# Kernel tuning notes

Hardware: AMD Instinct MI355X
Metric: run time of the kernel (lower is better)

The kernel has to match this reference:

```python
import jax, jax.numpy as jnp
import numpy as np

N, T, DIN, DH = 100000, 512, 256, 256


def setup_inputs() -> dict:
    key = jax.random.key(0)
    ks = jax.random.split(key, 7)
    s_in = 1.0 / np.sqrt(DH)  # torch GRU init scale
    X = jax.random.normal(ks[0], (N, DIN), dtype=jnp.float32)
    H = (jax.random.uniform(ks[1], (N, T)) < 0.02).astype(jnp.float32)
    W_ih = jax.random.uniform(ks[2], (3 * DH, DIN), minval=-s_in, maxval=s_in, dtype=jnp.float32)
    W_hh = jax.random.uniform(ks[3], (3 * DH, DH), minval=-s_in, maxval=s_in, dtype=jnp.float32)
    b_ih = jax.random.uniform(ks[4], (3 * DH,), minval=-s_in, maxval=s_in, dtype=jnp.float32)
    b_hh = jax.random.uniform(ks[5], (3 * DH,), minval=-s_in, maxval=s_in, dtype=jnp.float32)
    w_att = jax.random.uniform(ks[6], (DH,), minval=-s_in, maxval=s_in, dtype=jnp.float32)
    return {"X": X, "H": H, "W_ih": W_ih, "W_hh": W_hh, "b_ih": b_ih, "b_hh": b_hh, "w_att": w_att}


def _gru(visit_emb, W_ih, W_hh, b_ih, b_hh):
    # torch GRU gate order: r, z, n
    dh = W_hh.shape[1]
    gx = visit_emb @ W_ih.T + b_ih  # [T, 3H] precomputed input projections

    def step(h, gx_t):
        gh = h @ W_hh.T + b_hh  # [3H]
        r = jax.nn.sigmoid(gx_t[:dh] + gh[:dh])
        z = jax.nn.sigmoid(gx_t[dh:2 * dh] + gh[dh:2 * dh])
        n = jnp.tanh(gx_t[2 * dh:] + r * gh[2 * dh:])
        h_new = (1.0 - z) * n + z * h
        return h_new, h_new

    h0 = jnp.zeros((dh,), dtype=visit_emb.dtype)
    _, hs = jax.lax.scan(step, h0, gx)
    return hs  # [T, H]


def reference(X, H, W_ih, W_hh, b_ih, b_hh, w_att):
    visit_emb = H.T @ X  # [T, Din] incidence aggregation
    hidden = _gru(visit_emb, W_ih, W_hh, b_ih, b_hh)  # [T, H]
    alpha = jax.nn.softmax(hidden @ w_att, axis=0)  # [T]
    # diag(alpha) @ hidden summed over T == alpha-weighted sum
    return jnp.einsum("t,th->h", alpha, hidden)
```

## Files before the change

kernel.cpp:

```cpp
#include <hip/hip_runtime.h>
#include <hip/hip_bf16.h>

#define N_ROWS 100000
#define T_DIM  512
#define DIN    256
#define DH     256
#define KC     800
#define NSTEP  25
#define NCHUNK 125

typedef __attribute__((ext_vector_type(8))) short s16x8;
typedef __attribute__((ext_vector_type(4))) float f32x4;

static __device__ __forceinline__ unsigned bf16pair(float lo, float hi) {
  unsigned a = __builtin_bit_cast(unsigned, lo);
  unsigned b = __builtin_bit_cast(unsigned, hi);
  a = (a + 0x7fffu + ((a >> 16) & 1u)) >> 16;
  b = (b + 0x7fffu + ((b >> 16) & 1u)) & 0xffff0000u;
  return a | b;
}

__global__ __launch_bounds__(512, 2) void k_agg_mfma(
    const float* __restrict__ X, const float* __restrict__ Hm,
    float* __restrict__ ve, float* __restrict__ ve_part, int use_part)
{
  __shared__ unsigned smem[8192];
  const int tid  = threadIdx.x;
  const int mt   = blockIdx.x & 1;
  const int kc   = blockIdx.x >> 1;
  const int m0   = mt * 256;
  const int k0   = kc * KC;
  const int lane = tid & 63;
  const int wv   = tid >> 6;
  const int wm   = wv >> 2, wn = wv & 3;

  f32x4 acc[8][4] = {};

  const int kp0 = tid >> 6;
  const int kp1 = kp0 + 8;
  const int gg  = tid & 63;

  float4 ra0, ra1, ra2, ra3, rb0, rb1, rb2, rb3;

  auto load_tile = [&](int kt) {
    const size_t kb = (size_t)(k0 + kt * 32);
    const float* pa0 = &Hm[(kb + 2 * kp0) * T_DIM + m0 + gg * 4];
    ra0 = *(const float4*)pa0;
    ra1 = *(const float4*)(pa0 + T_DIM);
    const float* pa1 = &Hm[(kb + 2 * kp1) * T_DIM + m0 + gg * 4];
    ra2 = *(const float4*)pa1;
    ra3 = *(const float4*)(pa1 + T_DIM);
    const float* pb0 = &X[(kb + 2 * kp0) * DIN + gg * 4];
    rb0 = *(const float4*)pb0;
    rb1 = *(const float4*)(pb0 + DIN);
    const float* pb1 = &X[(kb + 2 * kp1) * DIN + gg * 4];
    rb2 = *(const float4*)pb1;
    rb3 = *(const float4*)(pb1 + DIN);
  };

  auto store_tile = [&]() {
#pragma unroll
    for (int d = 0; d < 4; ++d) {
      const int m  = gg * 4 + d;
      const int sw = d << 2;
      smem[m * 16 + (kp0 ^ sw)]        = bf16pair(((const float*)&ra0)[d], ((const float*)&ra1)[d]);
      smem[m * 16 + (kp1 ^ sw)]        = bf16pair(((const float*)&ra2)[d], ((const float*)&ra3)[d]);
      smem[4096 + m * 16 + (kp0 ^ sw)] = bf16pair(((const float*)&rb0)[d], ((const float*)&rb1)[d]);
      smem[4096 + m * 16 + (kp1 ^ sw)] = bf16pair(((const float*)&rb2)[d], ((const float*)&rb3)[d]);
    }
  };

  auto compute = [&]() {
    const uint4* sv = (const uint4*)smem;
    s16x8 af[8], bfr[4];
#pragma unroll
    for (int fm = 0; fm < 8; ++fm) {
      const int m = wm * 128 + fm * 16 + (lane & 15);
      af[fm] = __builtin_bit_cast(s16x8, sv[m * 4 + ((lane >> 4) ^ (m & 3))]);
    }
#pragma unroll
    for (int fn = 0; fn < 4; ++fn) {
      const int n = wn * 64 + fn * 16 + (lane & 15);
      bfr[fn] = __builtin_bit_cast(s16x8, sv[1024 + n * 4 + ((lane >> 4) ^ (n & 3))]);
    }
#pragma unroll
    for (int fm = 0; fm < 8; ++fm)
#pragma unroll
      for (int fn = 0; fn < 4; ++fn)
        acc[fm][fn] = __builtin_amdgcn_mfma_f32_16x16x32_bf16(af[fm], bfr[fn], acc[fm][fn], 0, 0, 0);
  };

  load_tile(0);
  store_tile();
  for (int kt = 0; kt < NSTEP; ++kt) {
    __syncthreads();
    if (kt + 1 < NSTEP) load_tile(kt + 1);
    compute();
    __syncthreads();
    if (kt + 1 < NSTEP) store_tile();
  }

  if (use_part) {
    float* dst = ve_part + (size_t)kc * (512 * 256);
#pragma unroll
    for (int fm = 0; fm < 8; ++fm) {
      const int r0 = m0 + wm * 128 + fm * 16 + (lane >> 4) * 4;
#pragma unroll
      for (int fn = 0; fn < 4; ++fn) {
        const int cc = wn * 64 + fn * 16 + (lane & 15);
#pragma unroll
        for (int q = 0; q < 4; ++q)
          dst[(size_t)(r0 + q) * 256 + cc] = acc[fm][fn][q];
      }
    }
  } else {
#pragma unroll
    for (int fm = 0; fm < 8; ++fm) {
      const int r0 = m0 + wm * 128 + fm * 16 + (lane >> 4) * 4;
#pragma unroll
      for (int fn = 0; fn < 4; ++fn) {
        const int cc = wn * 64 + fn * 16 + (lane & 15);
#pragma unroll
        for (int q = 0; q < 4; ++q)
          atomicAdd(&ve[(size_t)(r0 + q) * 256 + cc], acc[fm][fn][q]);
      }
    }
  }
}

__global__ __launch_bounds__(256) void k_gx(
    const float* __restrict__ vesrc, int npart,
    const float* __restrict__ Wih, const float* __restrict__ bih,
    float* __restrict__ gx)
{
  __shared__ float vl[DIN];
  const int t = blockIdx.x, j = threadIdx.x;
  float s = 0.f;
  for (int p = 0; p < npart; ++p) s += vesrc[(size_t)p * (512 * 256) + t * DIN + j];
  vl[j] = s;
  __syncthreads();
  float a0 = bih[j], a1 = bih[256 + j], a2 = bih[512 + j];
  const float* __restrict__ w0 = &Wih[(size_t)j * DIN];
  const float* __restrict__ w1 = &Wih[(size_t)(j + 256) * DIN];
  const float* __restrict__ w2 = &Wih[(size_t)(j + 512) * DIN];
#pragma unroll 4
  for (int k = 0; k < DIN; ++k) {
    const float v = vl[k];
    a0 = fmaf(w0[k], v, a0);
    a1 = fmaf(w1[k], v, a1);
    a2 = fmaf(w2[k], v, a2);
  }
  gx[t * 768 + j]       = a0;
  gx[t * 768 + 256 + j] = a1;
  gx[t * 768 + 512 + j] = a2;
}

__global__ __launch_bounds__(512, 2) __attribute__((amdgpu_waves_per_eu(2, 2)))
void k_gru_att(
    const float* __restrict__ Whh, const float* __restrict__ bhh,
    const float* __restrict__ gx, const float* __restrict__ watt,
    float* __restrict__ hs, float* __restrict__ out)
{
  __shared__ __hip_bfloat16 hb[DH];
  __shared__ float ghs[768];
  __shared__ float bsh[768];
  __shared__ float sc[T_DIM];
  __shared__ float red[2];

  const int tid = threadIdx.x;
  const int w   = tid >> 6;
  const int l   = tid & 63;
  const int lr  = l & 15;
  const int lg  = l >> 4;

  int rowbase[6];
  rowbase[0] = w * 32;       rowbase[1] = w * 32 + 16;
  rowbase[2] = 256 + w * 32; rowbase[3] = 256 + w * 32 + 16;
  rowbase[4] = 512 + w * 32; rowbase[5] = 512 + w * 32 + 16;

  s16x8 wf[6][8];
#pragma unroll
  for (int tt = 0; tt < 6; ++tt) {
    const float* rp = &Whh[(size_t)(rowbase[tt] + lr) * DH + lg * 8];
#pragma unroll
    for (int kb = 0; kb < 8; ++kb) {
      const float4 x0 = *(const float4*)(rp + kb * 32);
      const float4 x1 = *(const float4*)(rp + kb * 32 + 4);
      uint4 uu;
      uu.x = bf16pair(x0.x, x0.y);
      uu.y = bf16pair(x0.z, x0.w);
      uu.z = bf16pair(x1.x, x1.y);
      uu.w = bf16pair(x1.z, x1.w);
      wf[tt][kb] = __builtin_bit_cast(s16x8, uu);
    }
  }

  bsh[tid] = bhh[tid < 768 ? tid : 0];
  if (tid < 256) {
    bsh[512 + tid] = bhh[512 + tid];
    hb[tid] = __float2bfloat16(0.0f);
  }
  float h = 0.f;
  __syncthreads();

  for (int t = 0; t < T_DIM; ++t) {
    float gxr = 0.f, gxz = 0.f, gxn = 0.f;
    if (tid < 256) {
      gxr = gx[t * 768 + tid];
      gxz = gx[t * 768 + 256 + tid];
      gxn = gx[t * 768 + 512 + tid];
    }
    f32x4 acc[6];
#pragma unroll
    for (int tt = 0; tt < 6; ++tt)
      acc[tt] = *(const f32x4*)&bsh[rowbase[tt] + lg * 4];
#pragma unroll
    for (int kb = 0; kb < 8; ++kb) {
      const s16x8 bf = *(const s16x8*)((const char*)hb + kb * 64 + lg * 16);
#pragma unroll
      for (int tt = 0; tt < 6; ++tt)
        acc[tt] = __builtin_amdgcn_mfma_f32_16x16x32_bf16(wf[tt][kb], bf, acc[tt], 0, 0, 0);
    }
    if (lr == 0) {
#pragma unroll
      for (int tt = 0; tt < 6; ++tt)
        *(f32x4*)&ghs[rowbase[tt] + lg * 4] = acc[tt];
    }
    __syncthreads();
    if (tid < 256) {
      const float r = 1.f / (1.f + __expf(-(gxr + ghs[tid])));
      const float z = 1.f / (1.f + __expf(-(gxz + ghs[256 + tid])));
      const float pn = gxn + r * ghs[512 + tid];
      const float n = 2.f / (1.f + __expf(-2.f * pn)) - 1.f;
      h = (1.f - z) * n + z * h;
      hs[t * DH + tid] = h;
      hb[tid] = __float2bfloat16(h);
    }
    __syncthreads();
  }

  {
    const float* __restrict__ hr = &hs[tid * DH];
    float s = 0.f;
#pragma unroll 4
    for (int k = 0; k < DH; k += 4) {
      const float4 hv = *(const float4*)(hr + k);
      const float4 wv4 = *(const float4*)(watt + k);
      s = fmaf(hv.x, wv4.x, s); s = fmaf(hv.y, wv4.y, s);
      s = fmaf(hv.z, wv4.z, s); s = fmaf(hv.w, wv4.w, s);
    }
    sc[tid] = s;
  }
  __syncthreads();
  if (tid < 64) {
    float m = -1e30f;
#pragma unroll
    for (int i = 0; i < 8; ++i) m = fmaxf(m, sc[tid * 8 + i]);
#pragma unroll
    for (int off = 32; off > 0; off >>= 1) m = fmaxf(m, __shfl_down(m, off));
    if (tid == 0) red[0] = m;
  }
  __syncthreads();
  const float M = red[0];
  sc[tid] = __expf(sc[tid] - M);
  __syncthreads();
  if (tid < 64) {
    float s = 0.f;
#pragma unroll
    for (int i = 0; i < 8; ++i) s += sc[tid * 8 + i];
#pragma unroll
    for (int off = 32; off > 0; off >>= 1) s += __shfl_down(s, off);
    if (tid == 0) red[1] = s;
  }
  __syncthreads();
  const float inv = 1.f / red[1];
  {
    const int j = tid & 255, half = tid >> 8;
    float acc = 0.f;
    for (int t = half * 256; t < half * 256 + 256; ++t)
      acc = fmaf(sc[t], hs[t * DH + j], acc);
    bsh[half * 256 + j] = acc;
  }
  __syncthreads();
  if (tid < 256) out[tid] = (bsh[tid] + bsh[256 + tid]) * inv;
}

extern "C" void kernel_launch(void* const* d_in, const int* in_sizes, int n_in,
                              void* d_out, int out_size, void* d_ws, size_t ws_size,
                              hipStream_t stream) {
  const float* X    = (const float*)d_in[0];
  const float* H    = (const float*)d_in[1];
  const float* Wih  = (const float*)d_in[2];
  const float* Whh  = (const float*)d_in[3];
  const float* bih  = (const float*)d_in[4];
  const float* bhh  = (const float*)d_in[5];
  const float* watt = (const float*)d_in[6];
  float* out = (float*)d_out;

  char* ws = (char*)d_ws;
  float* gx      = (float*)ws;
  float* hs      = (float*)(ws + 1572864);
  float* ve      = (float*)(ws + 2097152);
  float* ve_part = (float*)(ws + 2621440);

  const size_t need_part = 2621440 + 65536000;
  const int use_part = (ws_size >= need_part) ? 1 : 0;

  if (!use_part)
    hipMemsetAsync(ve, 0, T_DIM * DIN * sizeof(float), stream);

  k_agg_mfma<<<2 * NCHUNK, 512, 0, stream>>>(X, H, ve, ve_part, use_part);
  k_gx<<<T_DIM, 256, 0, stream>>>(use_part ? ve_part : ve, use_part ? NCHUNK : 1,
                                  Wih, bih, gx);
  k_gru_att<<<1, 512, 0, stream>>>(Whh, bhh, gx, watt, hs, out);
}
```

Before: 1.030 ms.

## Shrink GRU recurrence block to 4 waves with 12 MFMA tiles each

The sequential GRU kernel now runs with 256 threads (4 waves) instead of 512. Each wave holds 12 bf16 weight tiles of W_hh in registers rather than 6, and every thread does the gate math, with no idle half-block. The goal is to cut barrier and synchronisation cost per timestep in the latency-bound 512-step loop and to give the compiler a one-wave-per-SIMD register budget. The trade-off is more serial MFMA work per wave per step and a larger register footprint, plus w_att is staged in shared memory for the attention epilogue.

Result: slower. 1.177 ms (+14.2%).

```diff
diff --git a/kernel.cpp b/kernel.cpp
--- a/kernel.cpp
+++ b/kernel.cpp
@@ -155,7 +155,8 @@
   gx[t * 768 + 512 + j] = a2;
 }
 
-__global__ __launch_bounds__(512, 2) __attribute__((amdgpu_waves_per_eu(2, 2)))
+__global__ __attribute__((amdgpu_flat_work_group_size(256, 256),
+                          amdgpu_waves_per_eu(1, 1)))
 void k_gru_att(
     const float* __restrict__ Whh, const float* __restrict__ bhh,
     const float* __restrict__ gx, const float* __restrict__ watt,
@@ -165,6 +166,7 @@
   __shared__ float ghs[768];
   __shared__ float bsh[768];
   __shared__ float sc[T_DIM];
+  __shared__ float wa[DH];
   __shared__ float red[2];
 
   const int tid = threadIdx.x;
@@ -173,61 +175,60 @@
   const int lr  = l & 15;
   const int lg  = l >> 4;
 
-  int rowbase[6];
-  rowbase[0] = w * 32;       rowbase[1] = w * 32 + 16;
-  rowbase[2] = 256 + w * 32; rowbase[3] = 256 + w * 32 + 16;
-  rowbase[4] = 512 + w * 32; rowbase[5] = 512 + w * 32 + 16;
-
-  s16x8 wf[6][8];
-#pragma unroll
-  for (int tt = 0; tt < 6; ++tt) {
-    const float* rp = &Whh[(size_t)(rowbase[tt] + lr) * DH + lg * 8];
-#pragma unroll
-    for (int kb = 0; kb < 8; ++kb) {
-      const float4 x0 = *(const float4*)(rp + kb * 32);
-      const float4 x1 = *(const float4*)(rp + kb * 32 + 4);
-      uint4 uu;
-      uu.x = bf16pair(x0.x, x0.y);
-      uu.y = bf16pair(x0.z, x0.w);
-      uu.z = bf16pair(x1.x, x1.y);
-      uu.w = bf16pair(x1.z, x1.w);
-      wf[tt][kb] = __builtin_bit_cast(s16x8, uu);
-    }
-  }
-
-  bsh[tid] = bhh[tid < 768 ? tid : 0];
-  if (tid < 256) {
-    bsh[512 + tid] = bhh[512 + tid];
-    hb[tid] = __float2bfloat16(0.0f);
-  }
+  s16x8 wf[12][8];
+#pragma unroll
+  for (int g = 0; g < 3; ++g) {
+#pragma unroll
+    for (int s = 0; s < 4; ++s) {
+      const float* rp = &Whh[(size_t)(g * 256 + w * 64 + s * 16 + lr) * DH + lg * 8];
+#pragma unroll
+      for (int kb = 0; kb < 8; ++kb) {
+        const float4 x0 = *(const float4*)(rp + kb * 32);
+        const float4 x1 = *(const float4*)(rp + kb * 32 + 4);
+        uint4 uu;
+        uu.x = bf16pair(x0.x, x0.y);
+        uu.y = bf16pair(x0.z, x0.w);
+        uu.z = bf16pair(x1.x, x1.y);
+        uu.w = bf16pair(x1.z, x1.w);
+        wf[g * 4 + s][kb] = __builtin_bit_cast(s16x8, uu);
+      }
+    }
+  }
+
+  bsh[tid] = bhh[tid];
+  bsh[256 + tid] = bhh[256 + tid];
+  bsh[512 + tid] = bhh[512 + tid];
+  hb[tid] = __float2bfloat16(0.0f);
+  wa[tid] = watt[tid];
   float h = 0.f;
   __syncthreads();
 
   for (int t = 0; t < T_DIM; ++t) {
-    float gxr = 0.f, gxz = 0.f, gxn = 0.f;
-    if (tid < 256) {
-      gxr = gx[t * 768 + tid];
-      gxz = gx[t * 768 + 256 + tid];
-      gxn = gx[t * 768 + 512 + tid];
-    }
-    f32x4 acc[6];
-#pragma unroll
-    for (int tt = 0; tt < 6; ++tt)
-      acc[tt] = *(const f32x4*)&bsh[rowbase[tt] + lg * 4];
+    const float gxr = gx[t * 768 + tid];
+    const float gxz = gx[t * 768 + 256 + tid];
+    const float gxn = gx[t * 768 + 512 + tid];
+    f32x4 acc[12];
+#pragma unroll
+    for (int g = 0; g < 3; ++g)
+#pragma unroll
+      for (int s = 0; s < 4; ++s)
+        acc[g * 4 + s] = *(const f32x4*)&bsh[g * 256 + w * 64 + s * 16 + lg * 4];
 #pragma unroll
     for (int kb = 0; kb < 8; ++kb) {
       const s16x8 bf = *(const s16x8*)((const char*)hb + kb * 64 + lg * 16);
 #pragma unroll
-      for (int tt = 0; tt < 6; ++tt)
+      for (int tt = 0; tt < 12; ++tt)
         acc[tt] = __builtin_amdgcn_mfma_f32_16x16x32_bf16(wf[tt][kb], bf, acc[tt], 0, 0, 0);
     }
     if (lr == 0) {
 #pragma unroll
-      for (int tt = 0; tt < 6; ++tt)
-        *(f32x4*)&ghs[rowbase[tt] + lg * 4] = acc[tt];
+      for (int g = 0; g < 3; ++g)
+#pragma unroll
+        for (int s = 0; s < 4; ++s)
+          *(f32x4*)&ghs[g * 256 + w * 64 + s * 16 + lg * 4] = acc[g * 4 + s];
     }
     __syncthreads();
-    if (tid < 256) {
+    {
       const float r = 1.f / (1.f + __expf(-(gxr + ghs[tid])));
       const float z = 1.f / (1.f + __expf(-(gxz + ghs[256 + tid])));
       const float pn = gxn + r * ghs[512 + tid];
@@ -239,17 +240,19 @@
     __syncthreads();
   }
 
-  {
-    const float* __restrict__ hr = &hs[tid * DH];
+#pragma unroll
+  for (int tt = 0; tt < 2; ++tt) {
+    const int t = tid + tt * 256;
+    const float* __restrict__ hr = &hs[(size_t)t * DH];
     float s = 0.f;
 #pragma unroll 4
     for (int k = 0; k < DH; k += 4) {
       const float4 hv = *(const float4*)(hr + k);
-      const float4 wv4 = *(const float4*)(watt + k);
+      const float4 wv4 = *(const float4*)(&wa[k]);
       s = fmaf(hv.x, wv4.x, s); s = fmaf(hv.y, wv4.y, s);
       s = fmaf(hv.z, wv4.z, s); s = fmaf(hv.w, wv4.w, s);
     }
-    sc[tid] = s;
+    sc[t] = s;
   }
   __syncthreads();
   if (tid < 64) {
@@ -263,6 +266,7 @@
   __syncthreads();
   const float M = red[0];
   sc[tid] = __expf(sc[tid] - M);
+  sc[tid + 256] = __expf(sc[tid + 256] - M);
   __syncthreads();
   if (tid < 64) {
     float s = 0.f;
@@ -274,15 +278,9 @@
   }
   __syncthreads();
   const float inv = 1.f / red[1];
-  {
-    const int j = tid & 255, half = tid >> 8;
-    float acc = 0.f;
-    for (int t = half * 256; t < half * 256 + 256; ++t)
-      acc = fmaf(sc[t], hs[t * DH + j], acc);
-    bsh[half * 256 + j] = acc;
-  }
-  __syncthreads();
-  if (tid < 256) out[tid] = (bsh[tid] + bsh[256 + tid]) * inv;
+  float a = 0.f;
+  for (int t = 0; t < T_DIM; ++t) a = fmaf(sc[t], hs[(size_t)t * DH + tid], a);
+  out[tid] = a * inv;
 }
 
 extern "C" void kernel_launch(void* const* d_in, const int* in_sizes, int n_in,
@@ -312,5 +310,5 @@
   k_agg_mfma<<<2 * NCHUNK, 512, 0, stream>>>(X, H, ve, ve_part, use_part);
   k_gx<<<T_DIM, 256, 0, stream>>>(use_part ? ve_part : ve, use_part ? NCHUNK : 1,
                                   Wih, bih, gx);
-  k_gru_att<<<1, 512, 0, stream>>>(Whh, bhh, gx, watt, hs, out);
-}
+  k_gru_att<<<1, 256, 0, stream>>>(Whh, bhh, gx, watt, hs, out);
+}
```
